# Performance work log

Hardware: AMD Instinct MI355X
Metric: run time of the kernel (lower is better)

The kernel has to match this reference:

```python
import jax, jax.numpy as jnp
import numpy as np

T = 3072          # num tokens
HID = 5120        # hidden_size
H = 16            # num_local_heads
DN = 128          # qk_nope_head_dim
DR = 64           # qk_rope_head_dim
DQK = DN + DR     # qk_head_dim = 192
DV = 128          # v_head_dim
Q_RANK = 1536     # q_lora_rank
KV_RANK = 512     # kv_lora_rank


def rmsnorm(x, w, eps=1e-6):
    var = jnp.mean(jnp.square(x), axis=-1, keepdims=True)
    return x * jax.lax.rsqrt(var + eps) * w


def apply_rope(x, cos, sin):
    # neox-style rotate-half; x [..., DR], cos/sin broadcastable [..., DR//2]
    x1, x2 = jnp.split(x, 2, axis=-1)
    return jnp.concatenate([x1 * cos - x2 * sin, x2 * cos + x1 * sin], axis=-1)


def setup_inputs() -> dict:
    key = jax.random.key(0)
    ks = jax.random.split(key, 8)
    s = 0.02
    positions = jnp.arange(T, dtype=jnp.int32)
    hidden_states = jax.random.normal(ks[0], (T, HID), dtype=jnp.float32)
    llama_4_scaling = jnp.ones((T, 1, 1), dtype=jnp.float32)
    w_q_a = jax.random.normal(ks[1], (HID, Q_RANK), dtype=jnp.float32) * s
    q_a_ln_w = jnp.ones((Q_RANK,), dtype=jnp.float32)
    w_q_b = jax.random.normal(ks[2], (Q_RANK, H * DQK), dtype=jnp.float32) * s
    w_kv_a = jax.random.normal(ks[3], (HID, KV_RANK + DR), dtype=jnp.float32) * s
    kv_a_ln_w = jnp.ones((KV_RANK,), dtype=jnp.float32)
    w_kv_b = jax.random.normal(ks[4], (KV_RANK, H * (DN + DV)), dtype=jnp.float32) * s
    w_o = jax.random.normal(ks[5], (H * DV, HID), dtype=jnp.float32) * s
    # cos/sin cache: [max_pos, DR]; first half cos, second half sin
    inv_freq = 1.0 / (10000.0 ** (jnp.arange(0, DR, 2, dtype=jnp.float32) / DR))
    t = jnp.arange(T, dtype=jnp.float32)
    freqs = t[:, None] * inv_freq[None, :]              # [T, DR//2]
    cos_sin_cache = jnp.concatenate([jnp.cos(freqs), jnp.sin(freqs)], axis=-1)
    return {
        "positions": positions, "hidden_states": hidden_states,
        "llama_4_scaling": llama_4_scaling,
        "w_q_a": w_q_a, "q_a_ln_w": q_a_ln_w, "w_q_b": w_q_b,
        "w_kv_a": w_kv_a, "kv_a_ln_w": kv_a_ln_w, "w_kv_b": w_kv_b,
        "w_o": w_o, "cos_sin_cache": cos_sin_cache,
    }


def reference(positions, hidden_states, llama_4_scaling, w_q_a, q_a_ln_w,
              w_q_b, w_kv_a, kv_a_ln_w, w_kv_b, w_o, cos_sin_cache):
    # ---- Q path: low-rank down/up projection with RMSNorm ----
    q = rmsnorm(hidden_states @ w_q_a, q_a_ln_w) @ w_q_b       # [T, H*DQK]
    q = q.reshape(T, H, DQK)
    q_nope, q_pe = q[..., :DN], q[..., DN:]                    # [T,H,DN],[T,H,DR]

    # ---- KV path: compressed latent + shared rope key ----
    latent = hidden_states @ w_kv_a                            # [T, KV_RANK+DR]
    kv_a = rmsnorm(latent[:, :KV_RANK], kv_a_ln_w)             # [T, KV_RANK]
    k_pe = latent[:, KV_RANK:]                                 # [T, DR] (shared across heads)
    kv = (kv_a @ w_kv_b).reshape(T, H, DN + DV)
    k_nope, v = kv[..., :DN], kv[..., DN:]                     # [T,H,DN],[T,H,DV]

    # ---- partial RoPE on the rope slices only ----
    cs = cos_sin_cache[positions]                              # [T, DR]
    cos, sin = cs[:, :DR // 2], cs[:, DR // 2:]
    q_pe = apply_rope(q_pe, cos[:, None, :], sin[:, None, :])
    k_pe = apply_rope(k_pe, cos, sin)

    q = jnp.concatenate([q_nope, q_pe], axis=-1)               # [T, H, DQK]
    k = jnp.concatenate(
        [k_nope, jnp.broadcast_to(k_pe[:, None, :], (T, H, DR))], axis=-1)

    q = q * llama_4_scaling

    # ---- causal attention (v is zero-padded to DQK in the original;
    #      the pad contributes zeros and is sliced off, so we skip it) ----
    scale = 1.0 / jnp.sqrt(jnp.float32(DQK))
    scores = jnp.einsum('qhd,khd->hqk', q, k) * scale          # [H, T, T]
    causal = positions[:, None] >= positions[None, :]
    scores = jnp.where(causal[None, :, :], scores, jnp.finfo(scores.dtype).min)
    probs = jax.nn.softmax(scores, axis=-1)
    attn = jnp.einsum('hqk,khd->qhd', probs, v)                # [T, H, DV]

    return attn.reshape(T, H * DV) @ w_o                       # [T, HID]
```

## Files before the change

kernel.cpp:

```cpp
#include <hip/hip_runtime.h>
#include <hip/hip_bf16.h>
#include <math.h>

#define T_TOK 3072
#define HID_D 5120
#define NH 16
#define DN 128
#define DR 64
#define DQK 192
#define DV 128
#define QRANK 1536
#define KVRANK 512
#define MERGED_N 2176

typedef __attribute__((ext_vector_type(8))) short short8;
typedef __attribute__((ext_vector_type(4))) float f32x4;
typedef unsigned short u16;

__device__ __forceinline__ u16 f2bf(float f) {
    unsigned int u = __float_as_uint(f);
    unsigned int lsb = (u >> 16) & 1;
    u += 0x7fffu + lsb;
    return (u16)(u >> 16);
}
__device__ __forceinline__ float bf2f(u16 v) {
    return __uint_as_float(((unsigned int)v) << 16);
}

__device__ __forceinline__ void gload_lds16(const u16* g, u16* l) {
    __builtin_amdgcn_global_load_lds((const __attribute__((address_space(1))) void*)g,
                                     (__attribute__((address_space(3))) void*)l, 16, 0, 0);
}

__global__ __launch_bounds__(256) void convert_bf_k(const float* __restrict__ x,
                                                    u16* __restrict__ y, int n4)
{
    const int i = blockIdx.x * 256 + threadIdx.x;
    if (i < n4) {
        float4 v = ((const float4*)x)[i];
        ushort4 o;
        o.x = f2bf(v.x); o.y = f2bf(v.y); o.z = f2bf(v.z); o.w = f2bf(v.w);
        ((ushort4*)y)[i] = o;
    }
}

__global__ __launch_bounds__(256) void transpose_conv_k(const float* __restrict__ W,
                                                        u16* __restrict__ WT,
                                                        int K, int N)
{
    __shared__ float tile[32][33];
    const int n0 = blockIdx.x * 32, k0 = blockIdx.y * 32;
    const int tx = threadIdx.x & 31, ty = threadIdx.x >> 5;
#pragma unroll
    for (int i = 0; i < 32; i += 8) {
        const int nn = n0 + tx;
        tile[ty + i][tx] = (nn < N) ? W[(size_t)(k0 + ty + i) * N + nn] : 0.f;
    }
    __syncthreads();
#pragma unroll
    for (int i = 0; i < 32; i += 8) {
        WT[(size_t)(n0 + ty + i) * K + k0 + tx] = f2bf(tile[tx][ty + i]);
    }
}

template <bool BF16_OUT>
__global__ __launch_bounds__(256) void bgemm_bt_k(
    const u16* __restrict__ A, const u16* __restrict__ BT, void* __restrict__ C,
    int Nreal, int K, int lda, int ldb, int ldc)
{
    __shared__ __attribute__((aligned(16))) u16 As[128 * 32];
    __shared__ __attribute__((aligned(16))) u16 Bs[128 * 32];

    const int tid  = threadIdx.x;
    const int wave = tid >> 6, lane = tid & 63;
    const int quad = lane >> 4, l16 = lane & 15;
    const int wr = (wave >> 1) * 64, wc = (wave & 1) * 64;

    const int gx  = (int)gridDim.x;
    const int nwg = gx * (int)gridDim.y;
    const int lin = (int)blockIdx.y * gx + (int)blockIdx.x;
    const int wid = (lin & 7) * (nwg >> 3) + (lin >> 3);
    const int row0 = (wid / gx) * 128, col0 = (wid % gx) * 128;

    f32x4 acc[4][4];
#pragma unroll
    for (int i = 0; i < 4; ++i)
#pragma unroll
        for (int j = 0; j < 4; ++j) acc[i][j] = (f32x4){0.f, 0.f, 0.f, 0.f};

    const int sr  = tid >> 2;
    const int skc = (tid & 3) * 8;
    const u16* ap0 = A  + (size_t)(row0 + sr)      * lda + skc;
    const u16* ap1 = A  + (size_t)(row0 + sr + 64) * lda + skc;
    const u16* bp0 = BT + (size_t)(col0 + sr)      * ldb + skc;
    const u16* bp1 = BT + (size_t)(col0 + sr + 64) * ldb + skc;
    u16* al0 = As + tid * 8;
    u16* al1 = As + tid * 8 + 64 * 32;
    u16* bl0 = Bs + tid * 8;
    u16* bl1 = Bs + tid * 8 + 64 * 32;

    for (int kt = 0; kt < K; kt += 32) {
        gload_lds16(ap0 + kt, al0);
        gload_lds16(ap1 + kt, al1);
        gload_lds16(bp0 + kt, bl0);
        gload_lds16(bp1 + kt, bl1);
        __syncthreads();

        short8 af[4], bf[4];
#pragma unroll
        for (int mi = 0; mi < 4; ++mi)
            af[mi] = *(const short8*)(As + (wr + mi * 16 + l16) * 32 + quad * 8);
#pragma unroll
        for (int ni = 0; ni < 4; ++ni)
            bf[ni] = *(const short8*)(Bs + (wc + ni * 16 + l16) * 32 + quad * 8);
#pragma unroll
        for (int mi = 0; mi < 4; ++mi)
#pragma unroll
            for (int ni = 0; ni < 4; ++ni)
                acc[mi][ni] = __builtin_amdgcn_mfma_f32_16x16x32_bf16(
                    af[mi], bf[ni], acc[mi][ni], 0, 0, 0);
        __syncthreads();
    }

#pragma unroll
    for (int mi = 0; mi < 4; ++mi) {
#pragma unroll
        for (int ni = 0; ni < 4; ++ni) {
            const int col_g = col0 + wc + ni * 16 + l16;
            if (col_g < Nreal) {
#pragma unroll
                for (int r = 0; r < 4; ++r) {
                    const int row_g = row0 + wr + mi * 16 + quad * 4 + r;
                    if (BF16_OUT)
                        ((u16*)C)[(size_t)row_g * ldc + col_g] = f2bf(acc[mi][ni][r]);
                    else
                        ((float*)C)[(size_t)row_g * ldc + col_g] = acc[mi][ni][r];
                }
            }
        }
    }
}

__global__ __launch_bounds__(256) void rmsnorm_bf_k(const u16* __restrict__ x,
                                                    const float* __restrict__ w,
                                                    u16* __restrict__ y,
                                                    int width, int stride, int off)
{
    const int row = blockIdx.x;
    const u16* xr = x + (size_t)row * stride + off;
    const int nch = width >> 3;
    float ss = 0.f;
    for (int i = threadIdx.x; i < nch; i += 256) {
        short8 v = *(const short8*)(xr + i * 8);
#pragma unroll
        for (int j = 0; j < 8; ++j) { const float f = bf2f((u16)v[j]); ss += f * f; }
    }
    __shared__ float red[256];
    red[threadIdx.x] = ss;
    __syncthreads();
    for (int s2 = 128; s2 > 0; s2 >>= 1) {
        if (threadIdx.x < s2) red[threadIdx.x] += red[threadIdx.x + s2];
        __syncthreads();
    }
    const float scale = rsqrtf(red[0] / (float)width + 1e-6f);
    u16* yr = y + (size_t)row * width;
    for (int i = threadIdx.x; i < nch; i += 256) {
        short8 v = *(const short8*)(xr + i * 8);
        const float4 w0 = *(const float4*)(w + i * 8);
        const float4 w1 = *(const float4*)(w + i * 8 + 4);
        short8 o;
        o[0] = (short)f2bf(bf2f((u16)v[0]) * scale * w0.x);
        o[1] = (short)f2bf(bf2f((u16)v[1]) * scale * w0.y);
        o[2] = (short)f2bf(bf2f((u16)v[2]) * scale * w0.z);
        o[3] = (short)f2bf(bf2f((u16)v[3]) * scale * w0.w);
        o[4] = (short)f2bf(bf2f((u16)v[4]) * scale * w1.x);
        o[5] = (short)f2bf(bf2f((u16)v[5]) * scale * w1.y);
        o[6] = (short)f2bf(bf2f((u16)v[6]) * scale * w1.z);
        o[7] = (short)f2bf(bf2f((u16)v[7]) * scale * w1.w);
        *(short8*)(yr + i * 8) = o;
    }
}

__global__ __launch_bounds__(256) void rope_scale_q_bf_k(const u16* __restrict__ q, const int* __restrict__ positions,
                                  const float* __restrict__ scaling,
                                  const float* __restrict__ cs_cache, u16* __restrict__ qb)
{
    const int t = blockIdx.x;
    const int pos = positions[t];
    const float* cs = cs_cache + (size_t)pos * DR;
    const float s = scaling[t];
    __shared__ float c_sh[32], s_sh[32];
    if (threadIdx.x < 32) {
        c_sh[threadIdx.x] = cs[threadIdx.x];
        s_sh[threadIdx.x] = cs[32 + threadIdx.x];
    }
    __syncthreads();
    const u16* qt = q + (size_t)t * NH * DQK;
    u16* qo = qb + (size_t)t * NH * DQK;
    for (int cc = threadIdx.x; cc < NH * 20; cc += 256) {
        const int hh = cc / 20, c = cc % 20;
        const u16* qr = qt + hh * DQK;
        u16* qw = qo + hh * DQK;
        if (c < 16) {
            short8 v = *(const short8*)(qr + c * 8);
            short8 o;
#pragma unroll
            for (int j = 0; j < 8; ++j) o[j] = (short)f2bf(bf2f((u16)v[j]) * s);
            *(short8*)(qw + c * 8) = o;
        } else {
            const int d0 = (c - 16) * 8;
            short8 x1 = *(const short8*)(qr + 128 + d0);
            short8 x2 = *(const short8*)(qr + 160 + d0);
            short8 o1, o2;
#pragma unroll
            for (int j = 0; j < 8; ++j) {
                const float a = bf2f((u16)x1[j]), b = bf2f((u16)x2[j]);
                const float cv = c_sh[d0 + j], sv = s_sh[d0 + j];
                o1[j] = (short)f2bf((a * cv - b * sv) * s);
                o2[j] = (short)f2bf((b * cv + a * sv) * s);
            }
            *(short8*)(qw + 128 + d0) = o1;
            *(short8*)(qw + 160 + d0) = o2;
        }
    }
}

__global__ void rope_k_bf_k(const u16* __restrict__ qa_lat, u16* __restrict__ kpe,
                            const int* __restrict__ positions,
                            const float* __restrict__ cs_cache)
{
    const int t = blockIdx.x;
    const int d = threadIdx.x;
    if (d >= 32) return;
    const int pos = positions[t];
    const float* cs = cs_cache + (size_t)pos * DR;
    const float c = cs[d], sn = cs[32 + d];
    const u16* lr = qa_lat + (size_t)t * MERGED_N + QRANK + KVRANK;
    const float x1 = bf2f(lr[d]), x2 = bf2f(lr[32 + d]);
    kpe[(size_t)t * DR + d]      = f2bf(x1 * c - x2 * sn);
    kpe[(size_t)t * DR + 32 + d] = f2bf(x2 * c + x1 * sn);
}

__global__ __launch_bounds__(256) void transpose_v_k(const u16* __restrict__ kvb,
                                                     u16* __restrict__ vt)
{
    __shared__ u16 tile[64][72];
    const int t0 = blockIdx.x * 64, d0 = blockIdx.y * 64, h = blockIdx.z;
    const int tid = threadIdx.x;
    for (int cc = tid; cc < 64 * 8; cc += 256) {
        const int row = cc >> 3, c = (cc & 7) * 8;
        *(short8*)&tile[row][c] =
            *(const short8*)(kvb + ((size_t)(t0 + row) * NH + h) * (DN + DV) + DN + d0 + c);
    }
    __syncthreads();
    for (int cc = tid; cc < 64 * 8; cc += 256) {
        const int drow = cc >> 3, c = (cc & 7) * 8;
        short8 s;
#pragma unroll
        for (int j = 0; j < 8; ++j) s[j] = tile[c + j][drow];
        *(short8*)(vt + ((size_t)h * DV + d0 + drow) * T_TOK + t0 + c) = s;
    }
}

#define ATT_BM 128
#define ATT_BN 128
__global__ __launch_bounds__(512) void attn_mfma_k(
    const u16* __restrict__ qb, const u16* __restrict__ kvb,
    const u16* __restrict__ kpeb, const u16* __restrict__ vt,
    u16* __restrict__ attnb)
{
    __shared__ u16 Ks[ATT_BN][140];
    __shared__ u16 Ps[8][16][72];

    const int tid  = threadIdx.x;
    const int wave = tid >> 6;
    const int lane = tid & 63;
    const int quad = lane >> 4;
    const int l16  = lane & 15;

    const int bid   = (int)blockIdx.x;
    const int chunk = bid & 7;
    const int local = bid >> 3;
    const int h     = chunk * 2 + (local & 1);
    const int qblk  = 23 - (local >> 1);
    const int q0    = qblk * ATT_BM;
    const int wrow0 = q0 + wave * 16;
    const int qrow  = wrow0 + l16;

    short8 qf[6];
    {
        const u16* qp = qb + ((size_t)qrow * NH + h) * DQK + quad * 8;
#pragma unroll
        for (int c = 0; c < 6; ++c)
            qf[c] = *(const short8*)(qp + c * 32);
    }

    const u16* gp[4];
    u16*       ld[4];
#pragma unroll
    for (int i = 0; i < 4; ++i) {
        const int cc = tid + 512 * i;
        const int row = cc >> 4, c = cc & 15;
        gp[i] = kvb + ((size_t)row * NH + h) * (DN + DV) + c * 8;
        ld[i] = &Ks[row][c * 8];
    }
    const size_t gst = (size_t)ATT_BN * NH * (DN + DV);

    f32x4 oacc[8];
#pragma unroll
    for (int t = 0; t < 8; ++t) oacc[t] = (f32x4){0.f, 0.f, 0.f, 0.f};
    float m_old[4], l_run[4];
#pragma unroll
    for (int r = 0; r < 4; ++r) { m_old[r] = -1e30f; l_run[r] = 0.f; }

    const u16* vbase = vt + ((size_t)h * DV + l16) * T_TOK + quad * 8;
    const int nkt = qblk + 1;

    short8 streg[4];
#pragma unroll
    for (int i = 0; i < 4; ++i) streg[i] = *(const short8*)gp[i];

    for (int kt = 0; kt < nkt; ++kt) {
        const int k0 = kt * ATT_BN;
        __syncthreads();
#pragma unroll
        for (int i = 0; i < 4; ++i) *(short8*)ld[i] = streg[i];
        if (kt + 1 < nkt) {
#pragma unroll
            for (int i = 0; i < 4; ++i)
                streg[i] = *(const short8*)(gp[i] + (size_t)(kt + 1) * gst);
        }
        __syncthreads();

#pragma unroll
        for (int half = 0; half < 2; ++half) {
            const int k0s = k0 + half * 64;
            if (k0s > wrow0 + 15) break;

            f32x4 sacc[4];
#pragma unroll
            for (int t = 0; t < 4; ++t) sacc[t] = (f32x4){0.f, 0.f, 0.f, 0.f};
#pragma unroll
            for (int t = 0; t < 4; ++t) {
                const int krow = k0s + t * 16 + l16;
                const u16* kp = &Ks[half * 64 + t * 16 + l16][quad * 8];
                const u16* pr = kpeb + (size_t)krow * DR + quad * 8;
                short8 b4 = *(const short8*)(pr);
                short8 b5 = *(const short8*)(pr + 32);
                sacc[t] = __builtin_amdgcn_mfma_f32_16x16x32_bf16(qf[0], *(const short8*)(kp),       sacc[t], 0, 0, 0);
                sacc[t] = __builtin_amdgcn_mfma_f32_16x16x32_bf16(qf[1], *(const short8*)(kp + 32),  sacc[t], 0, 0, 0);
                sacc[t] = __builtin_amdgcn_mfma_f32_16x16x32_bf16(qf[2], *(const short8*)(kp + 64),  sacc[t], 0, 0, 0);
                sacc[t] = __builtin_amdgcn_mfma_f32_16x16x32_bf16(qf[3], *(const short8*)(kp + 96),  sacc[t], 0, 0, 0);
                sacc[t] = __builtin_amdgcn_mfma_f32_16x16x32_bf16(qf[4], b4, sacc[t], 0, 0, 0);
                sacc[t] = __builtin_amdgcn_mfma_f32_16x16x32_bf16(qf[5], b5, sacc[t], 0, 0, 0);
            }
            short8 vv[8];
#pragma unroll
            for (int t = 0; t < 8; ++t)
                vv[t] = *(const short8*)(vbase + (size_t)t * 16 * T_TOK + k0s);

            const float sc = 0.07216878364870322f;
            const int rbase = wrow0 + quad * 4;
            if (k0s + 63 > wrow0) {
#pragma unroll
                for (int t = 0; t < 4; ++t) {
                    const int colg = k0s + t * 16 + l16;
#pragma unroll
                    for (int r = 0; r < 4; ++r) {
                        const float s = sacc[t][r] * sc;
                        sacc[t][r] = (rbase + r >= colg) ? s : -1e30f;
                    }
                }
            } else {
#pragma unroll
                for (int t = 0; t < 4; ++t)
#pragma unroll
                    for (int r = 0; r < 4; ++r) sacc[t][r] *= sc;
            }
            float alpha[4];
#pragma unroll
            for (int r = 0; r < 4; ++r) {
                float mx = fmaxf(fmaxf(sacc[0][r], sacc[1][r]), fmaxf(sacc[2][r], sacc[3][r]));
                mx = fmaxf(mx, __shfl_xor(mx, 1));
                mx = fmaxf(mx, __shfl_xor(mx, 2));
                mx = fmaxf(mx, __shfl_xor(mx, 4));
                mx = fmaxf(mx, __shfl_xor(mx, 8));
                const float mnew = fmaxf(m_old[r], mx);
                alpha[r] = __expf(m_old[r] - mnew);
                float sum = 0.f;
#pragma unroll
                for (int t = 0; t < 4; ++t) {
                    const float p = __expf(sacc[t][r] - mnew);
                    sacc[t][r] = p;
                    sum += p;
                }
                sum += __shfl_xor(sum, 1);
                sum += __shfl_xor(sum, 2);
                sum += __shfl_xor(sum, 4);
                sum += __shfl_xor(sum, 8);
                l_run[r] = l_run[r] * alpha[r] + sum;
                m_old[r] = mnew;
            }
#pragma unroll
            for (int t = 0; t < 4; ++t)
#pragma unroll
                for (int r = 0; r < 4; ++r)
                    Ps[wave][quad * 4 + r][t * 16 + l16] = f2bf(sacc[t][r]);
#pragma unroll
            for (int t = 0; t < 8; ++t)
#pragma unroll
                for (int r = 0; r < 4; ++r)
                    oacc[t][r] *= alpha[r];
            short8 pfrag0 = *(const short8*)&Ps[wave][l16][quad * 8];
            short8 ww[8];
#pragma unroll
            for (int t = 0; t < 8; ++t)
                ww[t] = *(const short8*)(vbase + (size_t)t * 16 * T_TOK + k0s + 32);
#pragma unroll
            for (int t = 0; t < 8; ++t)
                oacc[t] = __builtin_amdgcn_mfma_f32_16x16x32_bf16(pfrag0, vv[t], oacc[t], 0, 0, 0);
            short8 pfrag1 = *(const short8*)&Ps[wave][l16][32 + quad * 8];
#pragma unroll
            for (int t = 0; t < 8; ++t)
                oacc[t] = __builtin_amdgcn_mfma_f32_16x16x32_bf16(pfrag1, ww[t], oacc[t], 0, 0, 0);
        }
    }

#pragma unroll
    for (int r = 0; r < 4; ++r) {
        const float linv = 1.f / l_run[r];
        const int row_g = wrow0 + quad * 4 + r;
        u16* op = attnb + (size_t)row_g * (NH * DV) + h * DV;
#pragma unroll
        for (int t = 0; t < 8; ++t)
            op[t * 16 + l16] = f2bf(oacc[t][r] * linv);
    }
}

extern "C" void kernel_launch(void* const* d_in, const int* in_sizes, int n_in,
                              void* d_out, int out_size, void* d_ws, size_t ws_size,
                              hipStream_t stream)
{
    const int*   positions = (const int*)d_in[0];
    const float* hidden    = (const float*)d_in[1];
    const float* scaling   = (const float*)d_in[2];
    const float* w_q_a     = (const float*)d_in[3];
    const float* q_a_ln_w  = (const float*)d_in[4];
    const float* w_q_b     = (const float*)d_in[5];
    const float* w_kv_a    = (const float*)d_in[6];
    const float* kv_a_ln_w = (const float*)d_in[7];
    const float* w_kv_b    = (const float*)d_in[8];
    const float* w_o       = (const float*)d_in[9];
    const float* cs_cache  = (const float*)d_in[10];
    float* out = (float*)d_out;

    char* p = (char*)d_ws;
    auto alloc = [&](size_t bytes) { char* r = p; p += (bytes + 255) & ~(size_t)255; return r; };

    char* regH      = alloc((size_t)T_TOK * HID_D * 2);
    u16*  hidden_bf = (u16*)regH;
    u16*  qraw_bf   = (u16*)regH;
    char* regQ      = alloc((size_t)T_TOK * MERGED_N * 2 + (size_t)T_TOK * QRANK * 2);
    u16*  qa_lat    = (u16*)regQ;
    u16*  q_a_norm  = (u16*)(regQ + (size_t)T_TOK * MERGED_N * 2);
    u16*  qb        = (u16*)regQ;
    u16* kv_a_norm = (u16*)alloc((size_t)T_TOK * KVRANK * 2);
    u16* kpe_bf    = (u16*)alloc((size_t)T_TOK * DR * 2);
    u16* kv_bf     = (u16*)alloc((size_t)T_TOK * NH * (DN + DV) * 2);
    u16* vt        = (u16*)alloc((size_t)NH * DV * T_TOK * 2);
    u16* attnb     = (u16*)alloc((size_t)T_TOK * NH * DV * 2);
    u16* wqakva_bt = (u16*)alloc((size_t)MERGED_N * HID_D * 2);
    u16* wqb_bt    = (u16*)alloc((size_t)(NH * DQK) * QRANK * 2);
    u16* wkvb_bt   = (u16*)alloc((size_t)(NH * (DN + DV)) * KVRANK * 2);
    u16* wo_bt     = (u16*)alloc((size_t)HID_D * (NH * DV) * 2);

    const dim3 blk(256);

    convert_bf_k<<<dim3((T_TOK * HID_D / 4 + 255) / 256), blk, 0, stream>>>(
        hidden, hidden_bf, T_TOK * HID_D / 4);
    transpose_conv_k<<<dim3(QRANK / 32, HID_D / 32), blk, 0, stream>>>(
        w_q_a, wqakva_bt, HID_D, QRANK);
    transpose_conv_k<<<dim3(640 / 32, HID_D / 32), blk, 0, stream>>>(
        w_kv_a, wqakva_bt + (size_t)QRANK * HID_D, HID_D, KVRANK + DR);
    transpose_conv_k<<<dim3(NH * DQK / 32, QRANK / 32), blk, 0, stream>>>(w_q_b, wqb_bt, QRANK, NH * DQK);
    transpose_conv_k<<<dim3(NH * (DN + DV) / 32, KVRANK / 32), blk, 0, stream>>>(w_kv_b, wkvb_bt, KVRANK, NH * (DN + DV));
    transpose_conv_k<<<dim3(HID_D / 32, NH * DV / 32), blk, 0, stream>>>(w_o, wo_bt, NH * DV, HID_D);

    bgemm_bt_k<true><<<dim3(MERGED_N / 128, T_TOK / 128), blk, 0, stream>>>(
        hidden_bf, wqakva_bt, qa_lat, QRANK + KVRANK + DR, HID_D, HID_D, HID_D, MERGED_N);
    rope_k_bf_k<<<dim3(T_TOK), dim3(64), 0, stream>>>(qa_lat, kpe_bf, positions, cs_cache);
    rmsnorm_bf_k<<<dim3(T_TOK), blk, 0, stream>>>(qa_lat, q_a_ln_w, q_a_norm, QRANK, MERGED_N, 0);
    rmsnorm_bf_k<<<dim3(T_TOK), blk, 0, stream>>>(qa_lat, kv_a_ln_w, kv_a_norm, KVRANK, MERGED_N, QRANK);
    bgemm_bt_k<true><<<dim3(NH * DQK / 128, T_TOK / 128), blk, 0, stream>>>(
        q_a_norm, wqb_bt, qraw_bf, NH * DQK, QRANK, QRANK, QRANK, NH * DQK);
    rope_scale_q_bf_k<<<dim3(T_TOK), blk, 0, stream>>>(qraw_bf, positions, scaling, cs_cache, qb);
    bgemm_bt_k<true><<<dim3(NH * (DN + DV) / 128, T_TOK / 128), blk, 0, stream>>>(
        kv_a_norm, wkvb_bt, kv_bf, NH * (DN + DV), KVRANK, KVRANK, KVRANK, NH * (DN + DV));
    transpose_v_k<<<dim3(T_TOK / 64, DV / 64, NH), blk, 0, stream>>>(kv_bf, vt);
    attn_mfma_k<<<dim3(384), dim3(512), 0, stream>>>(qb, kv_bf, kpe_bf, vt, attnb);
    bgemm_bt_k<false><<<dim3(HID_D / 128, T_TOK / 128), blk, 0, stream>>>(
        attnb, wo_bt, out, HID_D, NH * DV, NH * DV, NH * DV, HID_D);
}
```

Before: 871.4 us.

## Double-buffer 64-row K tiles in LDS with k_pe staged and one barrier per step

```diff
diff --git a/kernel.cpp b/kernel.cpp
--- a/kernel.cpp
+++ b/kernel.cpp
@@ -263,13 +263,15 @@
 }
 
 #define ATT_BM 128
-#define ATT_BN 128
+#define ATT_BN 64
+#define KS_STRIDE 200
+#define KS_BUF (64 * KS_STRIDE)
 __global__ __launch_bounds__(512) void attn_mfma_k(
     const u16* __restrict__ qb, const u16* __restrict__ kvb,
     const u16* __restrict__ kpeb, const u16* __restrict__ vt,
     u16* __restrict__ attnb)
 {
-    __shared__ u16 Ks[ATT_BN][140];
+    __shared__ u16 Ks[2 * KS_BUF];
     __shared__ u16 Ps[8][16][72];
 
     const int tid  = threadIdx.x;
@@ -295,16 +297,26 @@
             qf[c] = *(const short8*)(qp + c * 32);
     }
 
-    const u16* gp[4];
-    u16*       ld[4];
-#pragma unroll
-    for (int i = 0; i < 4; ++i) {
-        const int cc = tid + 512 * i;
-        const int row = cc >> 4, c = cc & 15;
-        gp[i] = kvb + ((size_t)row * NH + h) * (DN + DV) + c * 8;
-        ld[i] = &Ks[row][c * 8];
-    }
-    const size_t gst = (size_t)ATT_BN * NH * (DN + DV);
+    const u16* gp0; const u16* gp1; const u16* gp2;
+    size_t gs0, gs1, gs2;
+    int lo0, lo1, lo2;
+    {
+        const int cc0 = tid,       r0 = cc0 / 24, c0 = cc0 % 24;
+        const int cc1 = tid + 512, r1 = cc1 / 24, c1 = cc1 % 24;
+        const int cc2 = tid + 1024, r2 = cc2 / 24, c2 = cc2 % 24;
+        gp0 = (c0 < 16) ? kvb + ((size_t)r0 * NH + h) * (DN + DV) + c0 * 8
+                        : kpeb + (size_t)r0 * DR + (c0 - 16) * 8;
+        gs0 = (c0 < 16) ? (size_t)ATT_BN * NH * (DN + DV) : (size_t)ATT_BN * DR;
+        lo0 = r0 * KS_STRIDE + c0 * 8;
+        gp1 = (c1 < 16) ? kvb + ((size_t)r1 * NH + h) * (DN + DV) + c1 * 8
+                        : kpeb + (size_t)r1 * DR + (c1 - 16) * 8;
+        gs1 = (c1 < 16) ? (size_t)ATT_BN * NH * (DN + DV) : (size_t)ATT_BN * DR;
+        lo1 = r1 * KS_STRIDE + c1 * 8;
+        gp2 = (c2 < 16) ? kvb + ((size_t)r2 * NH + h) * (DN + DV) + c2 * 8
+                        : kpeb + (size_t)r2 * DR + (c2 - 16) * 8;
+        gs2 = (c2 < 16) ? (size_t)ATT_BN * NH * (DN + DV) : (size_t)ATT_BN * DR;
+        lo2 = r2 * KS_STRIDE + c2 * 8;
+    }
 
     f32x4 oacc[8];
 #pragma unroll
@@ -314,57 +326,65 @@
     for (int r = 0; r < 4; ++r) { m_old[r] = -1e30f; l_run[r] = 0.f; }
 
     const u16* vbase = vt + ((size_t)h * DV + l16) * T_TOK + quad * 8;
-    const int nkt = qblk + 1;
-
-    short8 streg[4];
-#pragma unroll
-    for (int i = 0; i < 4; ++i) streg[i] = *(const short8*)gp[i];
-
+    const int nkt = 2 * (qblk + 1);
+
+    short8 s0 = *(const short8*)gp0;
+    short8 s1 = *(const short8*)gp1;
+    short8 s2 = *(const short8*)gp2;
+    asm volatile("s_waitcnt vmcnt(0)" ::: "memory");
+    *(short8*)(Ks + lo0) = s0;
+    *(short8*)(Ks + lo1) = s1;
+    *(short8*)(Ks + lo2) = s2;
+    s0 = *(const short8*)(gp0 + gs0);
+    s1 = *(const short8*)(gp1 + gs1);
+    s2 = *(const short8*)(gp2 + gs2);
+    asm volatile("s_waitcnt vmcnt(0) lgkmcnt(0)" ::: "memory");
+    __builtin_amdgcn_s_barrier();
+    __builtin_amdgcn_sched_barrier(0);
+
+    int cur = 0;
     for (int kt = 0; kt < nkt; ++kt) {
+        if (kt + 1 < nkt) {
+            u16* wp = Ks + (cur ^ 1) * KS_BUF;
+            *(short8*)(wp + lo0) = s0;
+            *(short8*)(wp + lo1) = s1;
+            *(short8*)(wp + lo2) = s2;
+        }
+        if (kt + 2 < nkt) {
+            const size_t o = (size_t)(kt + 2);
+            s0 = *(const short8*)(gp0 + o * gs0);
+            s1 = *(const short8*)(gp1 + o * gs1);
+            s2 = *(const short8*)(gp2 + o * gs2);
+        }
+
         const int k0 = kt * ATT_BN;
-        __syncthreads();
-#pragma unroll
-        for (int i = 0; i < 4; ++i) *(short8*)ld[i] = streg[i];
-        if (kt + 1 < nkt) {
-#pragma unroll
-            for (int i = 0; i < 4; ++i)
-                streg[i] = *(const short8*)(gp[i] + (size_t)(kt + 1) * gst);
-        }
-        __syncthreads();
-
-#pragma unroll
-        for (int half = 0; half < 2; ++half) {
-            const int k0s = k0 + half * 64;
-            if (k0s > wrow0 + 15) break;
-
+        if (k0 <= wrow0 + 15) {
+            const u16* kb = Ks + cur * KS_BUF;
             f32x4 sacc[4];
 #pragma unroll
             for (int t = 0; t < 4; ++t) sacc[t] = (f32x4){0.f, 0.f, 0.f, 0.f};
+            __builtin_amdgcn_s_setprio(1);
 #pragma unroll
             for (int t = 0; t < 4; ++t) {
-                const int krow = k0s + t * 16 + l16;
-                const u16* kp = &Ks[half * 64 + t * 16 + l16][quad * 8];
-                const u16* pr = kpeb + (size_t)krow * DR + quad * 8;
-                short8 b4 = *(const short8*)(pr);
-                short8 b5 = *(const short8*)(pr + 32);
-                sacc[t] = __builtin_amdgcn_mfma_f32_16x16x32_bf16(qf[0], *(const short8*)(kp),       sacc[t], 0, 0, 0);
-                sacc[t] = __builtin_amdgcn_mfma_f32_16x16x32_bf16(qf[1], *(const short8*)(kp + 32),  sacc[t], 0, 0, 0);
-                sacc[t] = __builtin_amdgcn_mfma_f32_16x16x32_bf16(qf[2], *(const short8*)(kp + 64),  sacc[t], 0, 0, 0);
-                sacc[t] = __builtin_amdgcn_mfma_f32_16x16x32_bf16(qf[3], *(const short8*)(kp + 96),  sacc[t], 0, 0, 0);
-                sacc[t] = __builtin_amdgcn_mfma_f32_16x16x32_bf16(qf[4], b4, sacc[t], 0, 0, 0);
-                sacc[t] = __builtin_amdgcn_mfma_f32_16x16x32_bf16(qf[5], b5, sacc[t], 0, 0, 0);
+                const u16* kp = kb + (t * 16 + l16) * KS_STRIDE + quad * 8;
+#pragma unroll
+                for (int c = 0; c < 6; ++c) {
+                    short8 bfrag = *(const short8*)(kp + c * 32);
+                    sacc[t] = __builtin_amdgcn_mfma_f32_16x16x32_bf16(qf[c], bfrag, sacc[t], 0, 0, 0);
+                }
             }
+            __builtin_amdgcn_s_setprio(0);
             short8 vv[8];
 #pragma unroll
             for (int t = 0; t < 8; ++t)
-                vv[t] = *(const short8*)(vbase + (size_t)t * 16 * T_TOK + k0s);
+                vv[t] = *(const short8*)(vbase + (size_t)t * 16 * T_TOK + k0);
 
             const float sc = 0.07216878364870322f;
             const int rbase = wrow0 + quad * 4;
-            if (k0s + 63 > wrow0) {
+            if (k0 + ATT_BN - 1 > wrow0) {
 #pragma unroll
                 for (int t = 0; t < 4; ++t) {
-                    const int colg = k0s + t * 16 + l16;
+                    const int colg = k0 + t * 16 + l16;
 #pragma unroll
                     for (int r = 0; r < 4; ++r) {
                         const float s = sacc[t][r] * sc;
@@ -406,24 +426,31 @@
 #pragma unroll
                 for (int r = 0; r < 4; ++r)
                     Ps[wave][quad * 4 + r][t * 16 + l16] = f2bf(sacc[t][r]);
+            short8 ww[8];
+#pragma unroll
+            for (int t = 0; t < 8; ++t)
+                ww[t] = *(const short8*)(vbase + (size_t)t * 16 * T_TOK + k0 + 32);
 #pragma unroll
             for (int t = 0; t < 8; ++t)
 #pragma unroll
                 for (int r = 0; r < 4; ++r)
                     oacc[t][r] *= alpha[r];
             short8 pfrag0 = *(const short8*)&Ps[wave][l16][quad * 8];
-            short8 ww[8];
-#pragma unroll
-            for (int t = 0; t < 8; ++t)
-                ww[t] = *(const short8*)(vbase + (size_t)t * 16 * T_TOK + k0s + 32);
+            short8 pfrag1 = *(const short8*)&Ps[wave][l16][32 + quad * 8];
+            __builtin_amdgcn_s_setprio(1);
 #pragma unroll
             for (int t = 0; t < 8; ++t)
                 oacc[t] = __builtin_amdgcn_mfma_f32_16x16x32_bf16(pfrag0, vv[t], oacc[t], 0, 0, 0);
-            short8 pfrag1 = *(const short8*)&Ps[wave][l16][32 + quad * 8];
 #pragma unroll
             for (int t = 0; t < 8; ++t)
                 oacc[t] = __builtin_amdgcn_mfma_f32_16x16x32_bf16(pfrag1, ww[t], oacc[t], 0, 0, 0);
+            __builtin_amdgcn_s_setprio(0);
         }
+
+        asm volatile("s_waitcnt vmcnt(0) lgkmcnt(0)" ::: "memory");
+        __builtin_amdgcn_s_barrier();
+        __builtin_amdgcn_sched_barrier(0);
+        cur ^= 1;
     }
 
 #pragma unroll
```

Result: faster. 770.2 us (-11.6%).

## Retile causal attention to 64-row blocks with LDS-staged k_pe and MFMA row sums

Applied to the files above, without the earlier changes.

```diff
diff --git a/kernel.cpp b/kernel.cpp
--- a/kernel.cpp
+++ b/kernel.cpp
@@ -262,15 +262,15 @@
     }
 }
 
-#define ATT_BM 128
-#define ATT_BN 128
-__global__ __launch_bounds__(512) void attn_mfma_k(
+#define ATT_BN 64
+#define KS_STRIDE 200
+__global__ __launch_bounds__(256) void attn_mfma_k(
     const u16* __restrict__ qb, const u16* __restrict__ kvb,
     const u16* __restrict__ kpeb, const u16* __restrict__ vt,
     u16* __restrict__ attnb)
 {
-    __shared__ u16 Ks[ATT_BN][140];
-    __shared__ u16 Ps[8][16][72];
+    __shared__ u16 Ks[64 * KS_STRIDE];
+    __shared__ u16 Ps[4][16][72];
 
     const int tid  = threadIdx.x;
     const int wave = tid >> 6;
@@ -282,8 +282,8 @@
     const int chunk = bid & 7;
     const int local = bid >> 3;
     const int h     = chunk * 2 + (local & 1);
-    const int qblk  = 23 - (local >> 1);
-    const int q0    = qblk * ATT_BM;
+    const int qblk  = 47 - (local >> 1);
+    const int q0    = qblk * 64;
     const int wrow0 = q0 + wave * 16;
     const int qrow  = wrow0 + l16;
 
@@ -295,140 +295,152 @@
             qf[c] = *(const short8*)(qp + c * 32);
     }
 
-    const u16* gp[4];
-    u16*       ld[4];
-#pragma unroll
-    for (int i = 0; i < 4; ++i) {
-        const int cc = tid + 512 * i;
-        const int row = cc >> 4, c = cc & 15;
-        gp[i] = kvb + ((size_t)row * NH + h) * (DN + DV) + c * 8;
-        ld[i] = &Ks[row][c * 8];
-    }
-    const size_t gst = (size_t)ATT_BN * NH * (DN + DV);
+    short8 ones;
+#pragma unroll
+    for (int j = 0; j < 8; ++j) ones[j] = (short)0x3F80;
+
+    const u16* gp[6];
+    size_t gs[6];
+    int lo[6];
+#pragma unroll
+    for (int i = 0; i < 6; ++i) {
+        const int cc = tid + 256 * i;
+        const int r = cc / 24, c = cc % 24;
+        if (c < 16) {
+            gp[i] = kvb + ((size_t)r * NH + h) * (DN + DV) + c * 8;
+            gs[i] = (size_t)ATT_BN * NH * (DN + DV);
+        } else {
+            gp[i] = kpeb + (size_t)r * DR + (c - 16) * 8;
+            gs[i] = (size_t)ATT_BN * DR;
+        }
+        lo[i] = r * KS_STRIDE + c * 8;
+    }
 
     f32x4 oacc[8];
 #pragma unroll
     for (int t = 0; t < 8; ++t) oacc[t] = (f32x4){0.f, 0.f, 0.f, 0.f};
-    float m_old[4], l_run[4];
-#pragma unroll
-    for (int r = 0; r < 4; ++r) { m_old[r] = -1e30f; l_run[r] = 0.f; }
+    f32x4 lacc = (f32x4){0.f, 0.f, 0.f, 0.f};
+    float m_old[4];
+#pragma unroll
+    for (int r = 0; r < 4; ++r) m_old[r] = -1e30f;
 
     const u16* vbase = vt + ((size_t)h * DV + l16) * T_TOK + quad * 8;
     const int nkt = qblk + 1;
 
-    short8 streg[4];
-#pragma unroll
-    for (int i = 0; i < 4; ++i) streg[i] = *(const short8*)gp[i];
+    short8 s[6];
+#pragma unroll
+    for (int i = 0; i < 6; ++i) s[i] = *(const short8*)gp[i];
+    asm volatile("s_waitcnt vmcnt(0)" ::: "memory");
+#pragma unroll
+    for (int i = 0; i < 6; ++i) *(short8*)(Ks + lo[i]) = s[i];
+    asm volatile("s_waitcnt lgkmcnt(0)" ::: "memory");
+    __builtin_amdgcn_s_barrier();
+    __builtin_amdgcn_sched_barrier(0);
 
     for (int kt = 0; kt < nkt; ++kt) {
+        if (kt + 1 < nkt) {
+            const size_t o = (size_t)(kt + 1);
+#pragma unroll
+            for (int i = 0; i < 6; ++i) s[i] = *(const short8*)(gp[i] + o * gs[i]);
+        }
+
         const int k0 = kt * ATT_BN;
-        __syncthreads();
-#pragma unroll
-        for (int i = 0; i < 4; ++i) *(short8*)ld[i] = streg[i];
+        f32x4 sacc[4];
+#pragma unroll
+        for (int t = 0; t < 4; ++t) sacc[t] = (f32x4){0.f, 0.f, 0.f, 0.f};
+        __builtin_amdgcn_s_setprio(1);
+#pragma unroll
+        for (int t = 0; t < 4; ++t) {
+            const u16* kp = Ks + (t * 16 + l16) * KS_STRIDE + quad * 8;
+#pragma unroll
+            for (int c = 0; c < 6; ++c) {
+                short8 bfrag = *(const short8*)(kp + c * 32);
+                sacc[t] = __builtin_amdgcn_mfma_f32_16x16x32_bf16(qf[c], bfrag, sacc[t], 0, 0, 0);
+            }
+        }
+        __builtin_amdgcn_s_setprio(0);
+        short8 vv[8];
+#pragma unroll
+        for (int t = 0; t < 8; ++t)
+            vv[t] = *(const short8*)(vbase + (size_t)t * 16 * T_TOK + k0);
+
+        const float sc2 = 0.104117555f;
+        const int rbase = wrow0 + quad * 4;
+        if (kt == nkt - 1) {
+#pragma unroll
+            for (int t = 0; t < 4; ++t) {
+                const int colg = k0 + t * 16 + l16;
+#pragma unroll
+                for (int r = 0; r < 4; ++r) {
+                    const float v = sacc[t][r] * sc2;
+                    sacc[t][r] = (rbase + r >= colg) ? v : -1e30f;
+                }
+            }
+        } else {
+#pragma unroll
+            for (int t = 0; t < 4; ++t)
+#pragma unroll
+                for (int r = 0; r < 4; ++r) sacc[t][r] *= sc2;
+        }
+        float alpha[4];
+#pragma unroll
+        for (int r = 0; r < 4; ++r) {
+            float mx = fmaxf(fmaxf(sacc[0][r], sacc[1][r]), fmaxf(sacc[2][r], sacc[3][r]));
+            mx = fmaxf(mx, __shfl_xor(mx, 1));
+            mx = fmaxf(mx, __shfl_xor(mx, 2));
+            mx = fmaxf(mx, __shfl_xor(mx, 4));
+            mx = fmaxf(mx, __shfl_xor(mx, 8));
+            const float mnew = fmaxf(m_old[r], mx);
+            alpha[r] = exp2f(m_old[r] - mnew);
+#pragma unroll
+            for (int t = 0; t < 4; ++t)
+                sacc[t][r] = exp2f(sacc[t][r] - mnew);
+            m_old[r] = mnew;
+        }
+#pragma unroll
+        for (int t = 0; t < 4; ++t)
+#pragma unroll
+            for (int r = 0; r < 4; ++r)
+                Ps[wave][quad * 4 + r][t * 16 + l16] = f2bf(sacc[t][r]);
+        short8 ww[8];
+#pragma unroll
+        for (int t = 0; t < 8; ++t)
+            ww[t] = *(const short8*)(vbase + (size_t)t * 16 * T_TOK + k0 + 32);
+#pragma unroll
+        for (int t = 0; t < 8; ++t)
+#pragma unroll
+            for (int r = 0; r < 4; ++r)
+                oacc[t][r] *= alpha[r];
+#pragma unroll
+        for (int r = 0; r < 4; ++r) lacc[r] *= alpha[r];
+        short8 pfrag0 = *(const short8*)&Ps[wave][l16][quad * 8];
+        short8 pfrag1 = *(const short8*)&Ps[wave][l16][32 + quad * 8];
+        __builtin_amdgcn_s_setprio(1);
+#pragma unroll
+        for (int t = 0; t < 8; ++t)
+            oacc[t] = __builtin_amdgcn_mfma_f32_16x16x32_bf16(pfrag0, vv[t], oacc[t], 0, 0, 0);
+        lacc = __builtin_amdgcn_mfma_f32_16x16x32_bf16(pfrag0, ones, lacc, 0, 0, 0);
+#pragma unroll
+        for (int t = 0; t < 8; ++t)
+            oacc[t] = __builtin_amdgcn_mfma_f32_16x16x32_bf16(pfrag1, ww[t], oacc[t], 0, 0, 0);
+        lacc = __builtin_amdgcn_mfma_f32_16x16x32_bf16(pfrag1, ones, lacc, 0, 0, 0);
+        __builtin_amdgcn_s_setprio(0);
+
+        asm volatile("s_waitcnt lgkmcnt(0)" ::: "memory");
+        __builtin_amdgcn_s_barrier();
         if (kt + 1 < nkt) {
-#pragma unroll
-            for (int i = 0; i < 4; ++i)
-                streg[i] = *(const short8*)(gp[i] + (size_t)(kt + 1) * gst);
-        }
-        __syncthreads();
-
-#pragma unroll
-        for (int half = 0; half < 2; ++half) {
-            const int k0s = k0 + half * 64;
-            if (k0s > wrow0 + 15) break;
-
-            f32x4 sacc[4];
-#pragma unroll
-            for (int t = 0; t < 4; ++t) sacc[t] = (f32x4){0.f, 0.f, 0.f, 0.f};
-#pragma unroll
-            for (int t = 0; t < 4; ++t) {
-                const int krow = k0s + t * 16 + l16;
-                const u16* kp = &Ks[half * 64 + t * 16 + l16][quad * 8];
-                const u16* pr = kpeb + (size_t)krow * DR + quad * 8;
-                short8 b4 = *(const short8*)(pr);
-                short8 b5 = *(const short8*)(pr + 32);
-                sacc[t] = __builtin_amdgcn_mfma_f32_16x16x32_bf16(qf[0], *(const short8*)(kp),       sacc[t], 0, 0, 0);
-                sacc[t] = __builtin_amdgcn_mfma_f32_16x16x32_bf16(qf[1], *(const short8*)(kp + 32),  sacc[t], 0, 0, 0);
-                sacc[t] = __builtin_amdgcn_mfma_f32_16x16x32_bf16(qf[2], *(const short8*)(kp + 64),  sacc[t], 0, 0, 0);
-                sacc[t] = __builtin_amdgcn_mfma_f32_16x16x32_bf16(qf[3], *(const short8*)(kp + 96),  sacc[t], 0, 0, 0);
-                sacc[t] = __builtin_amdgcn_mfma_f32_16x16x32_bf16(qf[4], b4, sacc[t], 0, 0, 0);
-                sacc[t] = __builtin_amdgcn_mfma_f32_16x16x32_bf16(qf[5], b5, sacc[t], 0, 0, 0);
-            }
-            short8 vv[8];
-#pragma unroll
-            for (int t = 0; t < 8; ++t)
-                vv[t] = *(const short8*)(vbase + (size_t)t * 16 * T_TOK + k0s);
-
-            const float sc = 0.07216878364870322f;
-            const int rbase = wrow0 + quad * 4;
-            if (k0s + 63 > wrow0) {
-#pragma unroll
-                for (int t = 0; t < 4; ++t) {
-                    const int colg = k0s + t * 16 + l16;
-#pragma unroll
-                    for (int r = 0; r < 4; ++r) {
-                        const float s = sacc[t][r] * sc;
-                        sacc[t][r] = (rbase + r >= colg) ? s : -1e30f;
-                    }
-                }
-            } else {
-#pragma unroll
-                for (int t = 0; t < 4; ++t)
-#pragma unroll
-                    for (int r = 0; r < 4; ++r) sacc[t][r] *= sc;
-            }
-            float alpha[4];
-#pragma unroll
-            for (int r = 0; r < 4; ++r) {
-                float mx = fmaxf(fmaxf(sacc[0][r], sacc[1][r]), fmaxf(sacc[2][r], sacc[3][r]));
-                mx = fmaxf(mx, __shfl_xor(mx, 1));
-                mx = fmaxf(mx, __shfl_xor(mx, 2));
-                mx = fmaxf(mx, __shfl_xor(mx, 4));
-                mx = fmaxf(mx, __shfl_xor(mx, 8));
-                const float mnew = fmaxf(m_old[r], mx);
-                alpha[r] = __expf(m_old[r] - mnew);
-                float sum = 0.f;
-#pragma unroll
-                for (int t = 0; t < 4; ++t) {
-                    const float p = __expf(sacc[t][r] - mnew);
-                    sacc[t][r] = p;
-                    sum += p;
-                }
-                sum += __shfl_xor(sum, 1);
-                sum += __shfl_xor(sum, 2);
-                sum += __shfl_xor(sum, 4);
-                sum += __shfl_xor(sum, 8);
-                l_run[r] = l_run[r] * alpha[r] + sum;
-                m_old[r] = mnew;
-            }
-#pragma unroll
-            for (int t = 0; t < 4; ++t)
-#pragma unroll
-                for (int r = 0; r < 4; ++r)
-                    Ps[wave][quad * 4 + r][t * 16 + l16] = f2bf(sacc[t][r]);
-#pragma unroll
-            for (int t = 0; t < 8; ++t)
-#pragma unroll
-                for (int r = 0; r < 4; ++r)
-                    oacc[t][r] *= alpha[r];
-            short8 pfrag0 = *(const short8*)&Ps[wave][l16][quad * 8];
-            short8 ww[8];
-#pragma unroll
-            for (int t = 0; t < 8; ++t)
-                ww[t] = *(const short8*)(vbase + (size_t)t * 16 * T_TOK + k0s + 32);
-#pragma unroll
-            for (int t = 0; t < 8; ++t)
-                oacc[t] = __builtin_amdgcn_mfma_f32_16x16x32_bf16(pfrag0, vv[t], oacc[t], 0, 0, 0);
-            short8 pfrag1 = *(const short8*)&Ps[wave][l16][32 + quad * 8];
-#pragma unroll
-            for (int t = 0; t < 8; ++t)
-                oacc[t] = __builtin_amdgcn_mfma_f32_16x16x32_bf16(pfrag1, ww[t], oacc[t], 0, 0, 0);
-        }
+            asm volatile("s_waitcnt vmcnt(0)" ::: "memory");
+#pragma unroll
+            for (int i = 0; i < 6; ++i) *(short8*)(Ks + lo[i]) = s[i];
+            asm volatile("s_waitcnt lgkmcnt(0)" ::: "memory");
+        }
+        __builtin_amdgcn_s_barrier();
+        __builtin_amdgcn_sched_barrier(0);
     }
 
 #pragma unroll
     for (int r = 0; r < 4; ++r) {
-        const float linv = 1.f / l_run[r];
+        const float linv = 1.f / lacc[r];
         const int row_g = wrow0 + quad * 4 + r;
         u16* op = attnb + (size_t)row_g * (NH * DV) + h * DV;
 #pragma unroll
@@ -497,7 +509,7 @@
     bgemm_bt_k<true><<<dim3(NH * (DN + DV) / 128, T_TOK / 128), blk, 0, stream>>>(
         kv_a_norm, wkvb_bt, kv_bf, NH * (DN + DV), KVRANK, KVRANK, KVRANK, NH * (DN + DV));
     transpose_v_k<<<dim3(T_TOK / 64, DV / 64, NH), blk, 0, stream>>>(kv_bf, vt);
-    attn_mfma_k<<<dim3(384), dim3(512), 0, stream>>>(qb, kv_bf, kpe_bf, vt, attnb);
+    attn_mfma_k<<<dim3(768), dim3(256), 0, stream>>>(qb, kv_bf, kpe_bf, vt, attnb);
     bgemm_bt_k<false><<<dim3(HID_D / 128, T_TOK / 128), blk, 0, stream>>>(
         attnb, wo_bt, out, HID_D, NH * DV, NH * DV, NH * DV, HID_D);
 }
```

Measured after the change: 805.5 us. -7.6%, faster.
